# Optimization experiments

Hardware: AMD Instinct MI355X
Metric: run time of the kernel (lower is better)

## Reference

```python
import jax, jax.numpy as jnp
import numpy as np

B, S, D, DFF = 4, 2048, 1024, 4096
EPS = 1e-5


def layernorm(x, gamma, beta):
    mu = jnp.mean(x, axis=-1, keepdims=True)
    var = jnp.var(x, axis=-1, keepdims=True)
    return (x - mu) * jax.lax.rsqrt(var + EPS) * gamma + beta


def attention(Q, K, V, causal):
    d_k = Q.shape[-1]
    scores = jnp.einsum('bqd,bkd->bqk', Q, K) / jnp.sqrt(jnp.asarray(d_k, Q.dtype))
    if causal:
        q_len, k_len = scores.shape[-2], scores.shape[-1]
        mask = jnp.tril(jnp.ones((q_len, k_len), dtype=bool))
        scores = jnp.where(mask[None], scores, jnp.asarray(-jnp.inf, scores.dtype))
    w = jax.nn.softmax(scores, axis=-1)
    return jnp.einsum('bqk,bkd->bqd', w, V)


def setup_inputs() -> dict:
    key = jax.random.key(0)
    ks = jax.random.split(key, 12)
    sd = 0.02
    return {
        'y': jax.random.normal(ks[0], (B, S, D), jnp.float32),
        'Z': jax.random.normal(ks[1], (B, S, D), jnp.float32),
        'w1': jax.random.normal(ks[2], (D, DFF), jnp.float32) * sd,
        'b1': jnp.zeros((DFF,), jnp.float32),
        'w2': jax.random.normal(ks[3], (DFF, D), jnp.float32) * sd,
        'b2': jnp.zeros((D,), jnp.float32),
        'g1': jnp.ones((D,), jnp.float32), 'beta1': jnp.zeros((D,), jnp.float32),
        'g2': jnp.ones((D,), jnp.float32), 'beta2': jnp.zeros((D,), jnp.float32),
        'g3': jnp.ones((D,), jnp.float32), 'beta3': jnp.zeros((D,), jnp.float32),
    }


def reference(y, Z, w1, b1, w2, b2, g1, beta1, g2, beta2, g3, beta3):
    # masked (causal) self-attention, single head over full d_model
    sa = attention(y, y, y, causal=True)
    y = layernorm(y + sa, g1, beta1)
    # cross-attention to encoder memory Z
    ca = attention(y, Z, Z, causal=False)
    y = layernorm(y + ca, g2, beta2)
    # position-wise FFN
    h = jax.nn.relu(jnp.einsum('bsd,df->bsf', y, w1) + b1)
    ff = jnp.einsum('bsf,fd->bsd', h, w2) + b2
    y = layernorm(y + ff, g3, beta3)
    return y
```

## Files before the change

### kernel.cpp

```cpp
#include <hip/hip_runtime.h>
#include <hip/hip_bf16.h>
#include <hip/hip_fp8.h>


#define Bb 4
#define Ss 2048
#define Dd 1024
#define Ff 4096

typedef __attribute__((ext_vector_type(4))) float f32x4;
typedef __attribute__((ext_vector_type(8))) short bf16x8;
typedef __attribute__((ext_vector_type(2))) long i64x2;
typedef __attribute__((ext_vector_type(8))) unsigned short u16x8;
typedef __attribute__((ext_vector_type(4))) unsigned short u16x4;

__device__ __forceinline__ unsigned short f2bf(float f) {
  unsigned u = __float_as_uint(f);
  u += 0x7FFFu + ((u >> 16) & 1u);
  return (unsigned short)(u >> 16);
}
__device__ __forceinline__ float bf2f(unsigned short h) {
  return __uint_as_float(((unsigned)h) << 16);
}
__device__ __forceinline__ unsigned char f2f8(float f) {
  __hip_fp8_e4m3 q(f);
  return q.__x;
}
__device__ __forceinline__ int f8col(int c) {
  int g = c >> 6, b = c & 63, o = b >> 3, j = b & 7;
  return g * 64 + (2 * (o & 3) + (o >> 2)) * 8 + j;
}

__device__ __forceinline__ void gload_lds16(const void* g, void* l) {
  __builtin_amdgcn_global_load_lds((const __attribute__((address_space(1))) void*)g,
                                   (__attribute__((address_space(3))) void*)l, 16, 0, 0);
}

__device__ __forceinline__ int xcd8(int orig, int n) {
  int q = n >> 3, r = n & 7;
  int x = orig & 7;
  int base = x < r ? x * (q + 1) : r * (q + 1) + (x - r) * q;
  return base + (orig >> 3);
}

__global__ __launch_bounds__(256) void k_transpose2(const float* __restrict__ inA,
                                                    const float* __restrict__ inB,
                                                    unsigned short* __restrict__ outTA,
                                                    unsigned short* __restrict__ outTB,
                                                    unsigned char* __restrict__ out8A,
                                                    unsigned char* __restrict__ out8B,
                                                    int R, int C) {
  __shared__ float t[32][33];
  int z = blockIdx.z;
  bool second = z >= Bb;
  int b = second ? z - Bb : z;
  size_t bo = (size_t)b * R * C;
  const float* pin = (second ? inB : inA) + bo;
  unsigned short* poutT = (second ? outTB : outTA) + bo;
  unsigned char* pout8 = (second ? out8B : out8A) + bo;
  int c0 = blockIdx.x * 32, r0 = blockIdx.y * 32;
  int tx = threadIdx.x, ty = threadIdx.y;
#pragma unroll
  for (int i = 0; i < 4; i++) {
    float v = pin[(size_t)(r0 + ty + i * 8) * C + c0 + tx];
    t[ty + i * 8][tx] = v;
    pout8[(size_t)(r0 + ty + i * 8) * C + f8col(c0 + tx)] = f2f8(v);
  }
  __syncthreads();
#pragma unroll
  for (int i = 0; i < 4; i++)
    poutT[(size_t)(c0 + ty + i * 8) * R + r0 + tx] = f2bf(t[tx][ty + i * 8]);
}

__global__ __launch_bounds__(256) void k_transpose_cast(const float* __restrict__ in,
                                                        unsigned short* __restrict__ outT,
                                                        int R, int C) {
  __shared__ float t[32][33];
  const float* pin = in;
  unsigned short* poutT = outT;
  int c0 = blockIdx.x * 32, r0 = blockIdx.y * 32;
  int tx = threadIdx.x, ty = threadIdx.y;
#pragma unroll
  for (int i = 0; i < 4; i++)
    t[ty + i * 8][tx] = pin[(size_t)(r0 + ty + i * 8) * C + c0 + tx];
  __syncthreads();
#pragma unroll
  for (int i = 0; i < 4; i++)
    poutT[(size_t)(c0 + ty + i * 8) * R + r0 + tx] = f2bf(t[tx][ty + i * 8]);
}

#define BAR() __builtin_amdgcn_s_barrier()
#define PRIO1() __builtin_amdgcn_s_setprio(1)
#define PRIO0() __builtin_amdgcn_s_setprio(0)

#define LDA8(arr, mh, bo)                                                       \
  {                                                                             \
    _Pragma("unroll") for (int j_ = 0; j_ < QM; ++j_) {                         \
      _Pragma("unroll") for (int kh_ = 0; kh_ < 2; ++kh_) {                     \
        arr[j_][kh_] =                                                          \
            *(const bf16x8*)(lds + (bo) + ((mh)*QM + j_) * 2048 + aof[kh_]);    \
      }                                                                         \
    }                                                                           \
  }

#define LDB8(arr, nh, bo)                                                       \
  {                                                                             \
    _Pragma("unroll") for (int n_ = 0; n_ < 2; ++n_) {                          \
      _Pragma("unroll") for (int kh_ = 0; kh_ < 2; ++kh_) {                     \
        arr[n_][kh_] =                                                          \
            *(const bf16x8*)(lds + (bo) + ((nh)*2 + n_) * 2048 + bof[kh_]);     \
      }                                                                         \
    }                                                                           \
  }

#define MMQ(aarr, barr, mh, nh)                                                 \
  {                                                                             \
    _Pragma("unroll") for (int j_ = 0; j_ < QM; ++j_) {                         \
      _Pragma("unroll") for (int n_ = 0; n_ < 2; ++n_) {                        \
        _Pragma("unroll") for (int kh_ = 0; kh_ < 2; ++kh_) {                   \
          acc[(mh)*QM + j_][(nh)*2 + n_] = __builtin_amdgcn_mfma_f32_16x16x32_bf16( \
              aarr[j_][kh_], barr[n_][kh_], acc[(mh)*QM + j_][(nh)*2 + n_], 0, 0, 0); \
        }                                                                       \
      }                                                                         \
    }                                                                           \
  }

#define LDAF8(arr, mh, bo)                                                      \
  {                                                                             \
    _Pragma("unroll") for (int j_ = 0; j_ < 4; ++j_)                            \
        arr[j_] = *(const i64x2*)(lds + (bo) + ((mh)*4 + j_) * 1024 + aofs);    \
  }
#define LDBF8(arr, nh, bo)                                                      \
  {                                                                             \
    _Pragma("unroll") for (int n_ = 0; n_ < 2; ++n_)                            \
        arr[n_] = *(const i64x2*)(lds + (bo) + ((nh)*2 + n_) * 1024 + bofs);    \
  }
#define MMQF8(aarr, barr, mh, nh)                                               \
  {                                                                             \
    _Pragma("unroll") for (int j_ = 0; j_ < 4; ++j_) {                          \
      _Pragma("unroll") for (int n_ = 0; n_ < 2; ++n_) {                        \
        _Pragma("unroll") for (int kh_ = 0; kh_ < 2; ++kh_) {                   \
          acc[(mh)*4 + j_][(nh)*2 + n_] = __builtin_amdgcn_mfma_f32_16x16x32_fp8_fp8( \
              aarr[j_][kh_], barr[n_][kh_], acc[(mh)*4 + j_][(nh)*2 + n_], 0, 0, 0);  \
        }                                                                       \
      }                                                                         \
    }                                                                           \
  }

#define EPILOGUE(MR_, WMS_)                                                     \
  {                                                                             \
    const int colb = j0 + wc * 64 + fr;                                         \
    const int rowb = i0 + wr * (WMS_) + (kq << 2);                              \
    const size_t cb = (size_t)bz * bsC;                                         \
    _Pragma("unroll") for (int m = 0; m < (MR_); ++m) {                         \
      _Pragma("unroll") for (int r = 0; r < 4; ++r) {                           \
        size_t ro = cb + (size_t)(rowb + m * 16 + r) * ldc;                     \
        _Pragma("unroll") for (int n = 0; n < 4; ++n) {                         \
          float v = acc[m][n][r];                                               \
          int col = colb + n * 16;                                              \
          if (EPI == 0) Cb[ro + col] = f2bf(v * scale);                         \
          else if (EPI == 2) Cb[ro + col] = f2bf(fmaxf(v + bias[col], 0.f));    \
          else if (EPI == 6) Cb[ro + col] = f2bf(v + bf2f(residB[ro + col]));   \
          else Cb[ro + col] = f2bf(v + bias[col] + bf2f(residB[ro + col]));     \
        }                                                                       \
      }                                                                         \
    }                                                                           \
  }

template <bool CAUSAL>
__global__ __launch_bounds__(512) void k_gemm8f8(
    const unsigned char* __restrict__ Ag, const unsigned char* __restrict__ Bg,
    unsigned short* __restrict__ Cb,
    int K, int lda, int ldb, int ldc, long bsA, long bsB, long bsC, float scale) {
  constexpr int ABYTES = 16384, BBYTES = 16384;
  __shared__ alignas(16) char lds[2 * ABYTES + 2 * BBYTES];

  int i0, j0;
  if (CAUSAL) {
    int t = xcd8(blockIdx.x, gridDim.x);
    int ti = (int)((sqrtf(8.f * t + 1.f) - 1.f) * 0.5f);
    while ((ti + 1) * (ti + 2) / 2 <= t) ++ti;
    while (ti * (ti + 1) / 2 > t) --ti;
    i0 = ti * 256;
    j0 = (t - ti * (ti + 1) / 2) * 256;
  } else {
    int lin = xcd8(blockIdx.y * gridDim.x + blockIdx.x, gridDim.x * gridDim.y);
    i0 = (lin / gridDim.x) * 256;
    j0 = (lin % gridDim.x) * 256;
  }
  int bz = blockIdx.z;
  Ag += (size_t)bz * bsA;
  Bg += (size_t)bz * bsB;

  const int nk = K / 64;
  const int niter = nk / 2;

  const int tid = threadIdx.x;
  const int w = tid >> 6, lane = tid & 63;
  const int wr = w >> 2, wc = w & 3;

  const int srow = tid >> 2;
  const int scs = (tid & 3) ^ ((tid >> 3) & 3);
  const unsigned char* As = Ag + (size_t)(i0 + srow) * lda + scs * 16;
  const unsigned char* Bs = Bg + (size_t)(j0 + srow) * ldb + scs * 16;

  auto stA = [&](int kt, int hf) {
    int ks = kt < nk ? kt : nk - 1;
    gload_lds16(As + (size_t)(hf * 128) * lda + ks * 64,
                lds + (kt & 1) * ABYTES + hf * 8192 + w * 1024);
  };
  auto stB = [&](int kt, int hf) {
    int ks = kt < nk ? kt : nk - 1;
    gload_lds16(Bs + (size_t)(hf * 128) * ldb + ks * 64,
                lds + 2 * ABYTES + (kt & 1) * BBYTES + hf * 8192 + w * 1024);
  };

  const int fr = lane & 15, kq = lane >> 4;
  const int rA = wr * 128 + fr;
  const int rB = wc * 64 + fr;
  const unsigned aofs = rA * 64 + ((kq ^ ((rA >> 1) & 3)) << 4);
  const unsigned bofs = rB * 64 + ((kq ^ ((rB >> 1) & 3)) << 4);
  constexpr int A0 = 0, A1 = ABYTES, B0 = 2 * ABYTES, B1 = 2 * ABYTES + BBYTES;

  f32x4 acc[8][4];
#pragma unroll
  for (int m = 0; m < 8; ++m)
#pragma unroll
    for (int n = 0; n < 4; ++n) acc[m][n] = (f32x4){0.f, 0.f, 0.f, 0.f};

  i64x2 a0[4], a1[4], b0[2], b1[2];

  stA(0, 0); stA(0, 1); stB(0, 0); stB(0, 1);
  stA(1, 0); stA(1, 1); stB(1, 0);
  asm volatile("s_waitcnt vmcnt(3)" ::: "memory");
  BAR();
  LDAF8(a0, 0, A0); LDBF8(b0, 0, B0);

  for (int t = 0; t < niter; ++t) {
    const int ka = 2 * t + 2, kb = 2 * t + 3;
    LDAF8(a1, 1, A0);
    stB(2 * t + 1, 1);
    BAR(); PRIO1(); MMQF8(a0, b0, 0, 0); PRIO0(); BAR();
    LDBF8(b1, 1, B0);
    stA(ka, 0);
    BAR(); PRIO1(); MMQF8(a1, b0, 1, 0); PRIO0(); BAR();
    stA(ka, 1);
    BAR(); PRIO1(); MMQF8(a0, b1, 0, 1); PRIO0(); BAR();
    stB(ka, 0);
    asm volatile("s_waitcnt vmcnt(3)" ::: "memory");
    BAR();
    LDAF8(a0, 0, A1); LDBF8(b0, 0, B1);
    PRIO1(); MMQF8(a1, b1, 1, 1); PRIO0(); BAR();
    LDAF8(a1, 1, A1);
    stB(ka, 1);
    BAR(); PRIO1(); MMQF8(a0, b0, 0, 0); PRIO0(); BAR();
    LDBF8(b1, 1, B1);
    stA(kb, 0);
    BAR(); PRIO1(); MMQF8(a1, b0, 1, 0); PRIO0(); BAR();
    stA(kb, 1);
    BAR(); PRIO1(); MMQF8(a0, b1, 0, 1); PRIO0(); BAR();
    stB(kb, 0);
    asm volatile("s_waitcnt vmcnt(3)" ::: "memory");
    BAR();
    LDAF8(a0, 0, A0); LDBF8(b0, 0, B0);
    PRIO1(); MMQF8(a1, b1, 1, 1); PRIO0(); BAR();
  }

  const int colb = j0 + wc * 64 + fr;
  const int rowb = i0 + wr * 128 + (kq << 2);
  const size_t cb = (size_t)bz * bsC;
#pragma unroll
  for (int m = 0; m < 8; ++m) {
#pragma unroll
    for (int r = 0; r < 4; ++r) {
      size_t ro = cb + (size_t)(rowb + m * 16 + r) * ldc;
#pragma unroll
      for (int n = 0; n < 4; ++n)
        Cb[ro + colb + n * 16] = f2bf(acc[m][n][r] * scale);
    }
  }
}

template <int EPI, bool CAUSAL>
__global__ __launch_bounds__(512) void k_gemm8(
    const unsigned short* __restrict__ Ag, const unsigned short* __restrict__ Bg,
    unsigned short* __restrict__ Cb,
    const float* __restrict__ bias, const unsigned short* __restrict__ residB,
    int K, int lda, int ldb, int ldc, long bsA, long bsB, long bsC, float scale) {
  constexpr int QM = 4;
  constexpr int ABYTES = 32768, BBYTES = 32768;
  __shared__ alignas(16) char lds[2 * ABYTES + 2 * BBYTES];

  int i0, j0;
  if (CAUSAL) {
    int t = xcd8(blockIdx.x, gridDim.x);
    int ti = (int)((sqrtf(8.f * t + 1.f) - 1.f) * 0.5f);
    while ((ti + 1) * (ti + 2) / 2 <= t) ++ti;
    while (ti * (ti + 1) / 2 > t) --ti;
    i0 = ti * 256;
    j0 = (t - ti * (ti + 1) / 2) * 256;
  } else {
    int lin = xcd8(blockIdx.y * gridDim.x + blockIdx.x, gridDim.x * gridDim.y);
    i0 = (lin / gridDim.x) * 256;
    j0 = (lin % gridDim.x) * 256;
  }
  int bz = blockIdx.z;
  Ag += (size_t)bz * bsA;
  Bg += (size_t)bz * bsB;

  const int nk = K / 64;
  const int niter = nk / 2;

  const int tid = threadIdx.x;
  const int w = tid >> 6, lane = tid & 63;
  const int wr = w >> 2, wc = w & 3;

  const int srow = (w << 3) + (lane >> 3);
  const int bcs = (lane & 7) ^ (lane >> 3);
  const unsigned short* As = Ag + (size_t)(i0 + srow) * lda + bcs * 8;
  const unsigned short* Bs = Bg + (size_t)(j0 + srow) * ldb + bcs * 8;
  char* ldsAw = lds + w * 1024;
  char* ldsBw = lds + 2 * ABYTES + w * 1024;

  auto stA = [&](int kt, int hf) {
    int ks = kt < nk ? kt : nk - 1;
#pragma unroll
    for (int l = 0; l < 2; ++l)
      gload_lds16(As + (size_t)(hf * 128 + l * 64) * lda + ks * 64,
                  ldsAw + (kt & 1) * ABYTES + hf * 128 * 128 + l * 8192);
  };
  auto stB = [&](int kt, int hf) {
    int ks = kt < nk ? kt : nk - 1;
#pragma unroll
    for (int l = 0; l < 2; ++l)
      gload_lds16(Bs + (size_t)(hf * 128 + l * 64) * ldb + ks * 64,
                  ldsBw + (kt & 1) * BBYTES + hf * 128 * 128 + l * 8192);
  };

  const int fr = lane & 15, kq = lane >> 4;
  const int rA = wr * 128 + fr;
  const int rB = wc * 64 + fr;
  unsigned aof[2], bof[2];
  aof[0] = rA * 128 + ((kq ^ (rA & 7)) << 4);
  aof[1] = rA * 128 + (((kq + 4) ^ (rA & 7)) << 4);
  bof[0] = 2 * ABYTES + rB * 128 + ((kq ^ (rB & 7)) << 4);
  bof[1] = 2 * ABYTES + rB * 128 + (((kq + 4) ^ (rB & 7)) << 4);
  constexpr int A0 = 0, A1 = ABYTES, B0 = 0, B1 = BBYTES;

  f32x4 acc[8][4];
#pragma unroll
  for (int m = 0; m < 8; ++m)
#pragma unroll
    for (int n = 0; n < 4; ++n) acc[m][n] = (f32x4){0.f, 0.f, 0.f, 0.f};

  bf16x8 a0[QM][2], a1[QM][2], b0[2][2], b1[2][2];

  stA(0, 0); stA(0, 1); stB(0, 0); stB(0, 1);
  stA(1, 0); stA(1, 1); stB(1, 0);
  asm volatile("s_waitcnt vmcnt(6)" ::: "memory");
  BAR();
  LDA8(a0, 0, A0); LDB8(b0, 0, B0);

  for (int t = 0; t < niter; ++t) {
    const int ka = 2 * t + 2, kb = 2 * t + 3;
    LDA8(a1, 1, A0);
    stB(2 * t + 1, 1);
    BAR(); PRIO1(); MMQ(a0, b0, 0, 0); PRIO0(); BAR();
    LDB8(b1, 1, B0);
    stA(ka, 0);
    BAR(); PRIO1(); MMQ(a1, b0, 1, 0); PRIO0(); BAR();
    stA(ka, 1);
    BAR(); PRIO1(); MMQ(a0, b1, 0, 1); PRIO0(); BAR();
    stB(ka, 0);
    asm volatile("s_waitcnt vmcnt(6)" ::: "memory");
    BAR();
    LDA8(a0, 0, A1); LDB8(b0, 0, B1);
    PRIO1(); MMQ(a1, b1, 1, 1); PRIO0(); BAR();
    LDA8(a1, 1, A1);
    stB(ka, 1);
    BAR(); PRIO1(); MMQ(a0, b0, 0, 0); PRIO0(); BAR();
    LDB8(b1, 1, B1);
    stA(kb, 0);
    BAR(); PRIO1(); MMQ(a1, b0, 1, 0); PRIO0(); BAR();
    stA(kb, 1);
    BAR(); PRIO1(); MMQ(a0, b1, 0, 1); PRIO0(); BAR();
    stB(kb, 0);
    asm volatile("s_waitcnt vmcnt(6)" ::: "memory");
    BAR();
    LDA8(a0, 0, A0); LDB8(b0, 0, B0);
    PRIO1(); MMQ(a1, b1, 1, 1); PRIO0(); BAR();
  }
  EPILOGUE(8, 128)
}

template <int EPI, bool KCAP>
__global__ __launch_bounds__(512) void k_gemm4(
    const unsigned short* __restrict__ Ag, const unsigned short* __restrict__ Bg,
    unsigned short* __restrict__ Cb,
    const float* __restrict__ bias, const unsigned short* __restrict__ residB,
    int K, int lda, int ldb, int ldc, long bsA, long bsB, long bsC, float scale) {
  constexpr int QM = 4;
  constexpr int ABYTES = 16384, BBYTES = 32768;
  __shared__ alignas(16) char lds[2 * ABYTES + 2 * BBYTES];

  int lin = xcd8(blockIdx.y * gridDim.x + blockIdx.x, gridDim.x * gridDim.y);
  int i0 = (lin / gridDim.x) * 128;
  int j0 = (lin % gridDim.x) * 256;
  int bz = blockIdx.z;
  Ag += (size_t)bz * bsA;
  Bg += (size_t)bz * bsB;

  int nk = K / 64;
  if (KCAP) {
    int cap = i0 / 64 + 2;
    nk = nk < cap ? nk : cap;
  }
  const int niter = nk / 2;

  const int tid = threadIdx.x;
  const int w = tid >> 6, lane = tid & 63;
  const int wr = w >> 2, wc = w & 3;

  const int srow = (w << 3) + (lane >> 3);
  const int bcs = (lane & 7) ^ (lane >> 3);
  const unsigned short* As = Ag + (size_t)(i0 + srow) * lda + bcs * 8;
  const unsigned short* Bs = Bg + (size_t)(j0 + srow) * ldb + bcs * 8;
  char* ldsAw = lds + w * 1024;
  char* ldsBw = lds + 2 * ABYTES + w * 1024;

  auto stA2 = [&](int kt) {
    int ks = kt < nk ? kt : nk - 1;
#pragma unroll
    for (int hf = 0; hf < 2; ++hf)
      gload_lds16(As + (size_t)(hf * 64) * lda + ks * 64,
                  ldsAw + (kt & 1) * ABYTES + hf * 64 * 128);
  };
  auto stBh = [&](int kt, int hf) {
    int ks = kt < nk ? kt : nk - 1;
#pragma unroll
    for (int l = 0; l < 2; ++l)
      gload_lds16(Bs + (size_t)(hf * 128 + l * 64) * ldb + ks * 64,
                  ldsBw + (kt & 1) * BBYTES + hf * 128 * 128 + l * 8192);
  };

  const int fr = lane & 15, kq = lane >> 4;
  const int rA = wr * 64 + fr;
  const int rB = wc * 64 + fr;
  unsigned aof[2], bof[2];
  aof[0] = rA * 128 + ((kq ^ (rA & 7)) << 4);
  aof[1] = rA * 128 + (((kq + 4) ^ (rA & 7)) << 4);
  bof[0] = 2 * ABYTES + rB * 128 + ((kq ^ (rB & 7)) << 4);
  bof[1] = 2 * ABYTES + rB * 128 + (((kq + 4) ^ (rB & 7)) << 4);
  constexpr int A0 = 0, A1 = ABYTES, B0 = 0, B1 = BBYTES;

  f32x4 acc[4][4];
#pragma unroll
  for (int m = 0; m < 4; ++m)
#pragma unroll
    for (int n = 0; n < 4; ++n) acc[m][n] = (f32x4){0.f, 0.f, 0.f, 0.f};

  bf16x8 a[QM][2], b0[2][2], b1[2][2];

  stA2(0); stBh(0, 0); stBh(0, 1);
  stA2(1); stBh(1, 0);
  asm volatile("s_waitcnt vmcnt(4)" ::: "memory");
  BAR();
  LDA8(a, 0, A0); LDB8(b0, 0, B0);

  for (int t = 0; t < niter; ++t) {
    const int ka = 2 * t + 2, kb = 2 * t + 3;
    LDB8(b1, 1, B0);
    stBh(2 * t + 1, 1);
    BAR(); PRIO1(); MMQ(a, b0, 0, 0); PRIO0(); BAR();
    stA2(ka); stBh(ka, 0);
    asm volatile("s_waitcnt vmcnt(4)" ::: "memory");
    BAR();
    PRIO1(); MMQ(a, b1, 0, 1); PRIO0();
    LDA8(a, 0, A1); LDB8(b0, 0, B1);
    BAR();
    LDB8(b1, 1, B1);
    stBh(ka, 1);
    BAR(); PRIO1(); MMQ(a, b0, 0, 0); PRIO0(); BAR();
    stA2(kb); stBh(kb, 0);
    asm volatile("s_waitcnt vmcnt(4)" ::: "memory");
    BAR();
    PRIO1(); MMQ(a, b1, 0, 1); PRIO0();
    LDA8(a, 0, A0); LDB8(b0, 0, B0);
    BAR();
  }
  EPILOGUE(4, 64)
}

__global__ __launch_bounds__(512) void k_pv1(
    const unsigned short* __restrict__ Ag, const unsigned short* __restrict__ Bg,
    unsigned short* __restrict__ C0, unsigned short* __restrict__ C1,
    const float* __restrict__ residF) {
  constexpr int QM = 4;
  constexpr int ABYTES = 16384, BBYTES = 32768;
  __shared__ alignas(16) char lds[2 * ABYTES + 2 * BBYTES];
  const int lda = Ss, ldb = Ss, ldc = Dd;

  const int xc = blockIdx.x & 3, kh = blockIdx.x >> 2;
  const int iy = blockIdx.y;
  const int i0 = iy * 128, j0 = xc * 256;
  const int bz = blockIdx.z;
  Ag += (size_t)bz * ((long)Ss * Ss);
  Bg += (size_t)bz * ((long)Dd * Ss);

  const int cap = 2 * iy + 2;
  const int nA = (iy + 2) & ~1;
  const int kbase = kh ? nA : 0;
  const int nkr = kh ? cap - nA : nA;
  const int niter = nkr / 2;

  const int tid = threadIdx.x;
  const int w = tid >> 6, lane = tid & 63;
  const int wr = w >> 2, wc = w & 3;

  const int srow = (w << 3) + (lane >> 3);
  const int bcs = (lane & 7) ^ (lane >> 3);
  const unsigned short* As = Ag + (size_t)(i0 + srow) * lda + bcs * 8;
  const unsigned short* Bs = Bg + (size_t)(j0 + srow) * ldb + bcs * 8;
  char* ldsAw = lds + w * 1024;
  char* ldsBw = lds + 2 * ABYTES + w * 1024;

  auto stA2 = [&](int kt) {
    int ks = kbase + (kt < nkr ? kt : (nkr > 0 ? nkr - 1 : 0));
#pragma unroll
    for (int hf = 0; hf < 2; ++hf)
      gload_lds16(As + (size_t)(hf * 64) * lda + ks * 64,
                  ldsAw + (kt & 1) * ABYTES + hf * 64 * 128);
  };
  auto stBh = [&](int kt, int hf) {
    int ks = kbase + (kt < nkr ? kt : (nkr > 0 ? nkr - 1 : 0));
#pragma unroll
    for (int l = 0; l < 2; ++l)
      gload_lds16(Bs + (size_t)(hf * 128 + l * 64) * ldb + ks * 64,
                  ldsBw + (kt & 1) * BBYTES + hf * 128 * 128 + l * 8192);
  };

  const int fr = lane & 15, kq = lane >> 4;
  const int rA = wr * 64 + fr;
  const int rB = wc * 64 + fr;
  unsigned aof[2], bof[2];
  aof[0] = rA * 128 + ((kq ^ (rA & 7)) << 4);
  aof[1] = rA * 128 + (((kq + 4) ^ (rA & 7)) << 4);
  bof[0] = 2 * ABYTES + rB * 128 + ((kq ^ (rB & 7)) << 4);
  bof[1] = 2 * ABYTES + rB * 128 + (((kq + 4) ^ (rB & 7)) << 4);
  constexpr int A0 = 0, A1 = ABYTES, B0 = 0, B1 = BBYTES;

  f32x4 acc[4][4];
#pragma unroll
  for (int m = 0; m < 4; ++m)
#pragma unroll
    for (int n = 0; n < 4; ++n) acc[m][n] = (f32x4){0.f, 0.f, 0.f, 0.f};

  bf16x8 a[QM][2], b0[2][2], b1[2][2];

  stA2(0); stBh(0, 0); stBh(0, 1);
  stA2(1); stBh(1, 0);
  asm volatile("s_waitcnt vmcnt(4)" ::: "memory");
  BAR();
  LDA8(a, 0, A0); LDB8(b0, 0, B0);

  for (int t = 0; t < niter; ++t) {
    const int ka = 2 * t + 2, kb = 2 * t + 3;
    LDB8(b1, 1, B0);
    stBh(2 * t + 1, 1);
    BAR(); PRIO1(); MMQ(a, b0, 0, 0); PRIO0(); BAR();
    stA2(ka); stBh(ka, 0);
    asm volatile("s_waitcnt vmcnt(4)" ::: "memory");
    BAR();
    PRIO1(); MMQ(a, b1, 0, 1); PRIO0();
    LDA8(a, 0, A1); LDB8(b0, 0, B1);
    BAR();
    LDB8(b1, 1, B1);
    stBh(ka, 1);
    BAR(); PRIO1(); MMQ(a, b0, 0, 0); PRIO0(); BAR();
    stA2(kb); stBh(kb, 0);
    asm volatile("s_waitcnt vmcnt(4)" ::: "memory");
    BAR();
    PRIO1(); MMQ(a, b1, 0, 1); PRIO0();
    LDA8(a, 0, A0); LDB8(b0, 0, B0);
    BAR();
  }

  const int colb = j0 + wc * 64 + fr;
  const int rowb = i0 + wr * 64 + (kq << 2);
  const size_t cb = (size_t)bz * ((long)Ss * Dd);
  unsigned short* Cb = kh ? C1 : C0;
#pragma unroll
  for (int m = 0; m < 4; ++m) {
#pragma unroll
    for (int r = 0; r < 4; ++r) {
      size_t ro = cb + (size_t)(rowb + m * 16 + r) * ldc;
#pragma unroll
      for (int n = 0; n < 4; ++n) {
        float v = acc[m][n][r];
        int col = colb + n * 16;
        if (kh == 0) Cb[ro + col] = f2bf(v + residF[ro + col]);
        else Cb[ro + col] = f2bf(v);
      }
    }
  }
}

template <bool CAUSAL>
__global__ __launch_bounds__(256) void k_softmax(unsigned short* __restrict__ scores) {
  int row = blockIdx.x;
  int i = row & (Ss - 1);
  unsigned short* src = scores + (size_t)row * Ss;
  int nv = CAUSAL ? i + 1 : Ss;
  int nb = CAUSAL ? ((i & ~127) + 128) : Ss;
  int t = threadIdx.x;
  int w = t >> 6, lane = t & 63;
  bool act = t * 8 < nb;
  float v[8];
  float mx = -1e30f;
  if (act) {
    u16x8 raw = *(const u16x8*)(src + t * 8);
#pragma unroll
    for (int k = 0; k < 8; k++) {
      int j = t * 8 + k;
      v[k] = (j < nv) ? bf2f(raw[k]) : -1e30f;
      mx = fmaxf(mx, v[k]);
    }
  } else {
#pragma unroll
    for (int k = 0; k < 8; k++) v[k] = -1e30f;
  }
#pragma unroll
  for (int o = 32; o; o >>= 1) mx = fmaxf(mx, __shfl_xor(mx, o));
  __shared__ float red[8];
  if (lane == 0) red[w] = mx;
  __syncthreads();
  mx = fmaxf(fmaxf(red[0], red[1]), fmaxf(red[2], red[3]));
  float sum = 0.f;
#pragma unroll
  for (int k = 0; k < 8; k++) {
    float e = (v[k] > -1e29f) ? __expf(v[k] - mx) : 0.f;
    v[k] = e;
    sum += e;
  }
#pragma unroll
  for (int o = 32; o; o >>= 1) sum += __shfl_xor(sum, o);
  if (lane == 0) red[4 + w] = sum;
  __syncthreads();
  sum = red[4] + red[5] + red[6] + red[7];
  float inv = 1.f / sum;
  if (act) {
    u16x8 r;
#pragma unroll
    for (int k = 0; k < 8; k++) r[k] = f2bf(v[k] * inv);
    *(u16x8*)(src + t * 8) = r;
  }
}

template <int OM>
__global__ __launch_bounds__(256) void k_ln(const unsigned short* __restrict__ a,
                                            const unsigned short* __restrict__ a2,
                                            const float* __restrict__ g,
                                            const float* __restrict__ be,
                                            float* __restrict__ outf,
                                            unsigned short* __restrict__ outb,
                                            unsigned char* __restrict__ out8) {
  int row = blockIdx.x;
  size_t o = (size_t)row * Dd;
  int t = threadIdx.x;
  u16x4 raw = *(const u16x4*)(a + o + t * 4);
  f32x4 x;
#pragma unroll
  for (int k = 0; k < 4; k++) x[k] = bf2f(raw[k]);
  if (a2) {
    u16x4 raw2 = *(const u16x4*)(a2 + o + t * 4);
#pragma unroll
    for (int k = 0; k < 4; k++) x[k] += bf2f(raw2[k]);
  }
  float s = x[0] + x[1] + x[2] + x[3];
  float q = x[0] * x[0] + x[1] * x[1] + x[2] * x[2] + x[3] * x[3];
  int w = t >> 6, lane = t & 63;
#pragma unroll
  for (int of = 32; of; of >>= 1) {
    s += __shfl_xor(s, of);
    q += __shfl_xor(q, of);
  }
  __shared__ float red[8];
  if (lane == 0) {
    red[w] = s;
    red[4 + w] = q;
  }
  __syncthreads();
  s = red[0] + red[1] + red[2] + red[3];
  q = red[4] + red[5] + red[6] + red[7];
  float mean = s * (1.f / Dd);
  float var = q * (1.f / Dd) - mean * mean;
  float rstd = rsqrtf(var + 1e-5f);
  f32x4 gv = *(const f32x4*)(g + t * 4);
  f32x4 bv = *(const f32x4*)(be + t * 4);
  f32x4 y;
#pragma unroll
  for (int k = 0; k < 4; k++) y[k] = (x[k] - mean) * rstd * gv[k] + bv[k];
  if (OM == 0) {
    *(f32x4*)(outf + o + t * 4) = y;
  } else {
    u16x4 r;
    r[0] = f2bf(y[0]); r[1] = f2bf(y[1]); r[2] = f2bf(y[2]); r[3] = f2bf(y[3]);
    *(u16x4*)(outb + o + t * 4) = r;
    if (OM == 2) {
      int cbyte = t * 4;
      int gq = cbyte >> 6, oo = (cbyte >> 3) & 7, j = cbyte & 7;
      int phys = gq * 64 + (2 * (oo & 3) + (oo >> 2)) * 8 + j;
      unsigned rr = (unsigned)f2f8(y[0]) | ((unsigned)f2f8(y[1]) << 8) |
                    ((unsigned)f2f8(y[2]) << 16) | ((unsigned)f2f8(y[3]) << 24);
      *(unsigned*)(out8 + (size_t)row * Dd + phys) = rr;
    }
  }
}

extern "C" void kernel_launch(void* const* d_in, const int* in_sizes, int n_in, void* d_out,
                              int out_size, void* d_ws, size_t ws_size, hipStream_t stream) {
  (void)in_sizes; (void)n_in; (void)out_size; (void)ws_size;
  const float* y   = (const float*)d_in[0];
  const float* Z   = (const float*)d_in[1];
  const float* w1  = (const float*)d_in[2];
  const float* b1  = (const float*)d_in[3];
  const float* w2  = (const float*)d_in[4];
  const float* b2  = (const float*)d_in[5];
  const float* g1  = (const float*)d_in[6];
  const float* be1 = (const float*)d_in[7];
  const float* g2  = (const float*)d_in[8];
  const float* be2 = (const float*)d_in[9];
  const float* g3  = (const float*)d_in[10];
  const float* be3 = (const float*)d_in[11];
  float* out = (float*)d_out;

  char* ws = (char*)d_ws;
  const size_t MB = 1024ull * 1024ull;
  unsigned short* T   = (unsigned short*)(ws);
  unsigned short* y1b = (unsigned short*)(ws);
  unsigned short* ffo = (unsigned short*)(ws);
  unsigned short* Zt  = (unsigned short*)(ws + 16 * MB);
  unsigned short* ybf = (unsigned short*)(ws + 32 * MB);
  unsigned short* w1t = (unsigned short*)(ws + 48 * MB);
  unsigned short* w2t = (unsigned short*)(ws + 56 * MB);
  unsigned short* sc  = (unsigned short*)(ws + 64 * MB);
  unsigned short* h   = (unsigned short*)(ws + 64 * MB);
  unsigned char* y8   = (unsigned char*)(ws + 96 * MB);
  unsigned char* Z8   = (unsigned char*)(ws + 104 * MB);
  unsigned char* y18  = (unsigned char*)(ws + 112 * MB);
  unsigned short* attnb  = (unsigned short*)d_out;
  unsigned short* attnb2 = (unsigned short*)((char*)d_out + 16 * MB);

  dim3 b256(256), b512(512);
  const float scl = 1.f / 32.f;
  const long SD = (long)Ss * Dd, SS = (long)Ss * Ss;

  k_transpose2<<<dim3(Dd / 32, Ss / 32, 2 * Bb), dim3(32, 8), 0, stream>>>(
      y, Z, T, Zt, y8, Z8, Ss, Dd);
  k_transpose_cast<<<dim3(Ff / 32, Dd / 32, 1), dim3(32, 8), 0, stream>>>(w1, w1t, Dd, Ff);
  k_transpose_cast<<<dim3(Dd / 32, Ff / 32, 1), dim3(32, 8), 0, stream>>>(w2, w2t, Ff, Dd);

  k_gemm8f8<true><<<dim3(36, 1, Bb), b512, 0, stream>>>(
      y8, y8, sc, Dd, Dd, Dd, Ss, SD, SD, SS, scl);
  k_softmax<true><<<dim3(Bb * Ss), b256, 0, stream>>>(sc);
  k_pv1<<<dim3(8, Ss / 128, Bb), b512, 0, stream>>>(sc, T, attnb, attnb2, y);
  k_ln<2><<<dim3(Bb * Ss), b256, 0, stream>>>(attnb, attnb2, g1, be1, nullptr, y1b, y18);

  k_gemm8f8<false><<<dim3(Ss / 256, Ss / 256, Bb), b512, 0, stream>>>(
      y18, Z8, sc, Dd, Dd, Dd, Ss, SD, SD, SS, scl);
  k_softmax<false><<<dim3(Bb * Ss), b256, 0, stream>>>(sc);
  k_gemm4<6, false><<<dim3(Dd / 256, Ss / 128, Bb), b512, 0, stream>>>(
      sc, Zt, attnb, nullptr, y1b, Ss, Ss, Ss, Dd, SS, SD, SD, 1.f);
  k_ln<1><<<dim3(Bb * Ss), b256, 0, stream>>>(attnb, nullptr, g2, be2, nullptr, ybf, nullptr);

  k_gemm8<2, false><<<dim3(Ff / 256, (Bb * Ss) / 256, 1), b512, 0, stream>>>(
      ybf, w1t, h, b1, nullptr, Dd, Dd, Dd, Ff, 0L, 0L, 0L, 1.f);
  k_gemm4<7, false><<<dim3(Dd / 256, (Bb * Ss) / 128, 1), b512, 0, stream>>>(
      h, w2t, ffo, b2, ybf, Ff, Ff, Ff, Dd, 0L, 0L, 0L, 1.f);
  k_ln<0><<<dim3(Bb * Ss), b256, 0, stream>>>(ffo, nullptr, g3, be3, out, nullptr, nullptr);
}
```

Measured before the change: 374.1 us.

## Load-balance causal PV GEMM by pairing complementary row blocks per workgroup

The causal P·V kernel previously split every 128-row block into two K-halves, giving 512 workgroups with very uneven triangular work. Now each workgroup handles row block iy together with row block 15-iy: the full prefix for rows of the lower half, or the first 16 K tiles plus the tail of the mirrored block. This gives 256 workgroups with roughly equal K length, and only rows in blocks 8 and above write a second partial. The layernorm adds that partial only for those rows. The transpose kernels are also unified into one kernel launched per tensor, and the unused KCAP path is removed from gemm4.

Measured after the change: 350.0 us. 6.4% less time.

```diff
diff --git a/kernel.cpp b/kernel.cpp
--- a/kernel.cpp
+++ b/kernel.cpp
@@ -43,46 +43,23 @@
   return base + (orig >> 3);
 }
 
-__global__ __launch_bounds__(256) void k_transpose2(const float* __restrict__ inA,
-                                                    const float* __restrict__ inB,
-                                                    unsigned short* __restrict__ outTA,
-                                                    unsigned short* __restrict__ outTB,
-                                                    unsigned char* __restrict__ out8A,
-                                                    unsigned char* __restrict__ out8B,
-                                                    int R, int C) {
+__global__ __launch_bounds__(256) void k_transpose_cast(const float* __restrict__ in,
+                                                        unsigned short* __restrict__ outT,
+                                                        unsigned char* __restrict__ out8,
+                                                        int R, int C) {
   __shared__ float t[32][33];
-  int z = blockIdx.z;
-  bool second = z >= Bb;
-  int b = second ? z - Bb : z;
-  size_t bo = (size_t)b * R * C;
-  const float* pin = (second ? inB : inA) + bo;
-  unsigned short* poutT = (second ? outTB : outTA) + bo;
-  unsigned char* pout8 = (second ? out8B : out8A) + bo;
+  size_t bo = (size_t)blockIdx.z * R * C;
+  const float* pin = in + bo;
+  unsigned short* poutT = outT + bo;
+  unsigned char* pout8 = out8 ? out8 + bo : nullptr;
   int c0 = blockIdx.x * 32, r0 = blockIdx.y * 32;
   int tx = threadIdx.x, ty = threadIdx.y;
 #pragma unroll
   for (int i = 0; i < 4; i++) {
     float v = pin[(size_t)(r0 + ty + i * 8) * C + c0 + tx];
     t[ty + i * 8][tx] = v;
-    pout8[(size_t)(r0 + ty + i * 8) * C + f8col(c0 + tx)] = f2f8(v);
-  }
-  __syncthreads();
-#pragma unroll
-  for (int i = 0; i < 4; i++)
-    poutT[(size_t)(c0 + ty + i * 8) * R + r0 + tx] = f2bf(t[tx][ty + i * 8]);
-}
-
-__global__ __launch_bounds__(256) void k_transpose_cast(const float* __restrict__ in,
-                                                        unsigned short* __restrict__ outT,
-                                                        int R, int C) {
-  __shared__ float t[32][33];
-  const float* pin = in;
-  unsigned short* poutT = outT;
-  int c0 = blockIdx.x * 32, r0 = blockIdx.y * 32;
-  int tx = threadIdx.x, ty = threadIdx.y;
-#pragma unroll
-  for (int i = 0; i < 4; i++)
-    t[ty + i * 8][tx] = pin[(size_t)(r0 + ty + i * 8) * C + c0 + tx];
+    if (pout8) pout8[(size_t)(r0 + ty + i * 8) * C + f8col(c0 + tx)] = f2f8(v);
+  }
   __syncthreads();
 #pragma unroll
   for (int i = 0; i < 4; i++)
@@ -393,7 +370,7 @@
   EPILOGUE(8, 128)
 }
 
-template <int EPI, bool KCAP>
+template <int EPI>
 __global__ __launch_bounds__(512) void k_gemm4(
     const unsigned short* __restrict__ Ag, const unsigned short* __restrict__ Bg,
     unsigned short* __restrict__ Cb,
@@ -410,11 +387,7 @@
   Ag += (size_t)bz * bsA;
   Bg += (size_t)bz * bsB;
 
-  int nk = K / 64;
-  if (KCAP) {
-    int cap = i0 / 64 + 2;
-    nk = nk < cap ? nk : cap;
-  }
+  const int nk = K / 64;
   const int niter = nk / 2;
 
   const int tid = threadIdx.x;
@@ -491,8 +464,8 @@
   EPILOGUE(4, 64)
 }
 
-__global__ __launch_bounds__(512) void k_pv1(
-    const unsigned short* __restrict__ Ag, const unsigned short* __restrict__ Bg,
+__global__ __launch_bounds__(512) void k_pv1b(
+    const unsigned short* __restrict__ Pg, const unsigned short* __restrict__ Vt,
     unsigned short* __restrict__ C0, unsigned short* __restrict__ C1,
     const float* __restrict__ residF) {
   constexpr int QM = 4;
@@ -500,44 +473,19 @@
   __shared__ alignas(16) char lds[2 * ABYTES + 2 * BBYTES];
   const int lda = Ss, ldb = Ss, ldc = Dd;
 
-  const int xc = blockIdx.x & 3, kh = blockIdx.x >> 2;
-  const int iy = blockIdx.y;
-  const int i0 = iy * 128, j0 = xc * 256;
-  const int bz = blockIdx.z;
-  Ag += (size_t)bz * ((long)Ss * Ss);
-  Bg += (size_t)bz * ((long)Dd * Ss);
-
-  const int cap = 2 * iy + 2;
-  const int nA = (iy + 2) & ~1;
-  const int kbase = kh ? nA : 0;
-  const int nkr = kh ? cap - nA : nA;
-  const int niter = nkr / 2;
+  const int xc = blockIdx.x, iy = blockIdx.y, bz = blockIdx.z;
+  const int j0 = xc * 256;
+  const unsigned short* Ag0 = Pg + (size_t)bz * ((long)Ss * Ss);
+  const unsigned short* Bg = Vt + (size_t)bz * ((long)Dd * Ss);
 
   const int tid = threadIdx.x;
   const int w = tid >> 6, lane = tid & 63;
   const int wr = w >> 2, wc = w & 3;
-
   const int srow = (w << 3) + (lane >> 3);
   const int bcs = (lane & 7) ^ (lane >> 3);
-  const unsigned short* As = Ag + (size_t)(i0 + srow) * lda + bcs * 8;
   const unsigned short* Bs = Bg + (size_t)(j0 + srow) * ldb + bcs * 8;
   char* ldsAw = lds + w * 1024;
   char* ldsBw = lds + 2 * ABYTES + w * 1024;
-
-  auto stA2 = [&](int kt) {
-    int ks = kbase + (kt < nkr ? kt : (nkr > 0 ? nkr - 1 : 0));
-#pragma unroll
-    for (int hf = 0; hf < 2; ++hf)
-      gload_lds16(As + (size_t)(hf * 64) * lda + ks * 64,
-                  ldsAw + (kt & 1) * ABYTES + hf * 64 * 128);
-  };
-  auto stBh = [&](int kt, int hf) {
-    int ks = kbase + (kt < nkr ? kt : (nkr > 0 ? nkr - 1 : 0));
-#pragma unroll
-    for (int l = 0; l < 2; ++l)
-      gload_lds16(Bs + (size_t)(hf * 128 + l * 64) * ldb + ks * 64,
-                  ldsBw + (kt & 1) * BBYTES + hf * 128 * 128 + l * 8192);
-  };
 
   const int fr = lane & 15, kq = lane >> 4;
   const int rA = wr * 64 + fr;
@@ -549,59 +497,86 @@
   bof[1] = 2 * ABYTES + rB * 128 + (((kq + 4) ^ (rB & 7)) << 4);
   constexpr int A0 = 0, A1 = ABYTES, B0 = 0, B1 = BBYTES;
 
-  f32x4 acc[4][4];
-#pragma unroll
-  for (int m = 0; m < 4; ++m)
-#pragma unroll
-    for (int n = 0; n < 4; ++n) acc[m][n] = (f32x4){0.f, 0.f, 0.f, 0.f};
-
-  bf16x8 a[QM][2], b0[2][2], b1[2][2];
-
-  stA2(0); stBh(0, 0); stBh(0, 1);
-  stA2(1); stBh(1, 0);
-  asm volatile("s_waitcnt vmcnt(4)" ::: "memory");
-  BAR();
-  LDA8(a, 0, A0); LDB8(b0, 0, B0);
-
-  for (int t = 0; t < niter; ++t) {
-    const int ka = 2 * t + 2, kb = 2 * t + 3;
-    LDB8(b1, 1, B0);
-    stBh(2 * t + 1, 1);
-    BAR(); PRIO1(); MMQ(a, b0, 0, 0); PRIO0(); BAR();
-    stA2(ka); stBh(ka, 0);
+  auto runGemm = [&](int i0, int kbase, int nkr, unsigned short* Cb, bool addres) {
+    asm volatile("s_waitcnt vmcnt(0) lgkmcnt(0)" ::: "memory");
+    BAR();
+    const unsigned short* As = Ag0 + (size_t)(i0 + srow) * lda + bcs * 8;
+    auto stA2 = [&](int kt) {
+      int ks = kbase + (kt < nkr ? kt : nkr - 1);
+#pragma unroll
+      for (int hf = 0; hf < 2; ++hf)
+        gload_lds16(As + (size_t)(hf * 64) * lda + ks * 64,
+                    ldsAw + (kt & 1) * ABYTES + hf * 64 * 128);
+    };
+    auto stBh = [&](int kt, int hf) {
+      int ks = kbase + (kt < nkr ? kt : nkr - 1);
+#pragma unroll
+      for (int l = 0; l < 2; ++l)
+        gload_lds16(Bs + (size_t)(hf * 128 + l * 64) * ldb + ks * 64,
+                    ldsBw + (kt & 1) * BBYTES + hf * 128 * 128 + l * 8192);
+    };
+
+    f32x4 acc[4][4];
+#pragma unroll
+    for (int m = 0; m < 4; ++m)
+#pragma unroll
+      for (int n = 0; n < 4; ++n) acc[m][n] = (f32x4){0.f, 0.f, 0.f, 0.f};
+    bf16x8 a[QM][2], b0[2][2], b1[2][2];
+
+    stA2(0); stBh(0, 0); stBh(0, 1);
+    stA2(1); stBh(1, 0);
     asm volatile("s_waitcnt vmcnt(4)" ::: "memory");
     BAR();
-    PRIO1(); MMQ(a, b1, 0, 1); PRIO0();
-    LDA8(a, 0, A1); LDB8(b0, 0, B1);
-    BAR();
-    LDB8(b1, 1, B1);
-    stBh(ka, 1);
-    BAR(); PRIO1(); MMQ(a, b0, 0, 0); PRIO0(); BAR();
-    stA2(kb); stBh(kb, 0);
-    asm volatile("s_waitcnt vmcnt(4)" ::: "memory");
-    BAR();
-    PRIO1(); MMQ(a, b1, 0, 1); PRIO0();
     LDA8(a, 0, A0); LDB8(b0, 0, B0);
-    BAR();
-  }
-
-  const int colb = j0 + wc * 64 + fr;
-  const int rowb = i0 + wr * 64 + (kq << 2);
-  const size_t cb = (size_t)bz * ((long)Ss * Dd);
-  unsigned short* Cb = kh ? C1 : C0;
-#pragma unroll
-  for (int m = 0; m < 4; ++m) {
-#pragma unroll
-    for (int r = 0; r < 4; ++r) {
-      size_t ro = cb + (size_t)(rowb + m * 16 + r) * ldc;
-#pragma unroll
-      for (int n = 0; n < 4; ++n) {
-        float v = acc[m][n][r];
-        int col = colb + n * 16;
-        if (kh == 0) Cb[ro + col] = f2bf(v + residF[ro + col]);
-        else Cb[ro + col] = f2bf(v);
+
+    const int niter = nkr / 2;
+    for (int t = 0; t < niter; ++t) {
+      const int ka = 2 * t + 2, kb = 2 * t + 3;
+      LDB8(b1, 1, B0);
+      stBh(2 * t + 1, 1);
+      BAR(); PRIO1(); MMQ(a, b0, 0, 0); PRIO0(); BAR();
+      stA2(ka); stBh(ka, 0);
+      asm volatile("s_waitcnt vmcnt(4)" ::: "memory");
+      BAR();
+      PRIO1(); MMQ(a, b1, 0, 1); PRIO0();
+      LDA8(a, 0, A1); LDB8(b0, 0, B1);
+      BAR();
+      LDB8(b1, 1, B1);
+      stBh(ka, 1);
+      BAR(); PRIO1(); MMQ(a, b0, 0, 0); PRIO0(); BAR();
+      stA2(kb); stBh(kb, 0);
+      asm volatile("s_waitcnt vmcnt(4)" ::: "memory");
+      BAR();
+      PRIO1(); MMQ(a, b1, 0, 1); PRIO0();
+      LDA8(a, 0, A0); LDB8(b0, 0, B0);
+      BAR();
+    }
+
+    const int colb = j0 + wc * 64 + fr;
+    const int rowb = i0 + wr * 64 + (kq << 2);
+    const size_t cb = (size_t)bz * ((long)Ss * Dd);
+#pragma unroll
+    for (int m = 0; m < 4; ++m) {
+#pragma unroll
+      for (int r = 0; r < 4; ++r) {
+        size_t ro = cb + (size_t)(rowb + m * 16 + r) * ldc;
+#pragma unroll
+        for (int n = 0; n < 4; ++n) {
+          float v = acc[m][n][r];
+          int col = colb + n * 16;
+          if (addres) Cb[ro + col] = f2bf(v + residF[ro + col]);
+          else Cb[ro + col] = f2bf(v);
+        }
       }
     }
+  };
+
+  if (iy >= 8) {
+    runGemm(iy * 128, 0, 16, C0, true);
+  } else {
+    runGemm(iy * 128, 0, 2 * iy + 2, C0, true);
+    const int jy = 15 - iy;
+    runGemm(jy * 128, 16, 2 * jy - 14, C1, false);
   }
 }
 
@@ -671,7 +646,7 @@
   f32x4 x;
 #pragma unroll
   for (int k = 0; k < 4; k++) x[k] = bf2f(raw[k]);
-  if (a2) {
+  if (a2 && ((row & (Ss - 1)) >> 7) >= 8) {
     u16x4 raw2 = *(const u16x4*)(a2 + o + t * 4);
 #pragma unroll
     for (int k = 0; k < 4; k++) x[k] += bf2f(raw2[k]);
@@ -755,27 +730,27 @@
   const float scl = 1.f / 32.f;
   const long SD = (long)Ss * Dd, SS = (long)Ss * Ss;
 
-  k_transpose2<<<dim3(Dd / 32, Ss / 32, 2 * Bb), dim3(32, 8), 0, stream>>>(
-      y, Z, T, Zt, y8, Z8, Ss, Dd);
-  k_transpose_cast<<<dim3(Ff / 32, Dd / 32, 1), dim3(32, 8), 0, stream>>>(w1, w1t, Dd, Ff);
-  k_transpose_cast<<<dim3(Dd / 32, Ff / 32, 1), dim3(32, 8), 0, stream>>>(w2, w2t, Ff, Dd);
+  k_transpose_cast<<<dim3(Dd / 32, Ss / 32, Bb), dim3(32, 8), 0, stream>>>(y, T, y8, Ss, Dd);
+  k_transpose_cast<<<dim3(Dd / 32, Ss / 32, Bb), dim3(32, 8), 0, stream>>>(Z, Zt, Z8, Ss, Dd);
+  k_transpose_cast<<<dim3(Ff / 32, Dd / 32, 1), dim3(32, 8), 0, stream>>>(w1, w1t, nullptr, Dd, Ff);
+  k_transpose_cast<<<dim3(Dd / 32, Ff / 32, 1), dim3(32, 8), 0, stream>>>(w2, w2t, nullptr, Ff, Dd);
 
   k_gemm8f8<true><<<dim3(36, 1, Bb), b512, 0, stream>>>(
       y8, y8, sc, Dd, Dd, Dd, Ss, SD, SD, SS, scl);
   k_softmax<true><<<dim3(Bb * Ss), b256, 0, stream>>>(sc);
-  k_pv1<<<dim3(8, Ss / 128, Bb), b512, 0, stream>>>(sc, T, attnb, attnb2, y);
+  k_pv1b<<<dim3(4, 16, Bb), b512, 0, stream>>>(sc, T, attnb, attnb2, y);
   k_ln<2><<<dim3(Bb * Ss), b256, 0, stream>>>(attnb, attnb2, g1, be1, nullptr, y1b, y18);
 
   k_gemm8f8<false><<<dim3(Ss / 256, Ss / 256, Bb), b512, 0, stream>>>(
       y18, Z8, sc, Dd, Dd, Dd, Ss, SD, SD, SS, scl);
   k_softmax<false><<<dim3(Bb * Ss), b256, 0, stream>>>(sc);
-  k_gemm4<6, false><<<dim3(Dd / 256, Ss / 128, Bb), b512, 0, stream>>>(
+  k_gemm4<6><<<dim3(Dd / 256, Ss / 128, Bb), b512, 0, stream>>>(
       sc, Zt, attnb, nullptr, y1b, Ss, Ss, Ss, Dd, SS, SD, SD, 1.f);
   k_ln<1><<<dim3(Bb * Ss), b256, 0, stream>>>(attnb, nullptr, g2, be2, nullptr, ybf, nullptr);
 
   k_gemm8<2, false><<<dim3(Ff / 256, (Bb * Ss) / 256, 1), b512, 0, stream>>>(
       ybf, w1t, h, b1, nullptr, Dd, Dd, Dd, Ff, 0L, 0L, 0L, 1.f);
-  k_gemm4<7, false><<<dim3(Dd / 256, (Bb * Ss) / 128, 1), b512, 0, stream>>>(
+  k_gemm4<7><<<dim3(Dd / 256, (Bb * Ss) / 128, 1), b512, 0, stream>>>(
       h, w2t, ffo, b2, ybf, Ff, Ff, Ff, Dd, 0L, 0L, 0L, 1.f);
   k_ln<0><<<dim3(Bb * Ss), b256, 0, stream>>>(ffo, nullptr, g3, be3, out, nullptr, nullptr);
 }
```
